# Performance work log

Hardware: AMD Instinct MI355X
Metric: run time of the kernel (lower is better)

## Reference

```python
import jax, jax.numpy as jnp
import numpy as np

B, N, F_IN, F_OUT = 16, 1024, 256, 256
ALPHA = 0.2  # leakyrelu negative slope
NEG_BIG = -9e15


def setup_inputs() -> dict:
    key = jax.random.key(0)
    k1, k2, k3, k4 = jax.random.split(key, 4)
    h = jax.random.normal(k1, (B, N, F_IN), dtype=jnp.float32)
    adj = jax.random.randint(k2, (B, N, N), 0, 2, dtype=jnp.int32)
    # xavier_uniform with gain=1.414
    def xavier(k, shape, gain=1.414):
        fan_in, fan_out = shape[0], shape[1]
        bound = gain * np.sqrt(6.0 / (fan_in + fan_out))
        return jax.random.uniform(k, shape, dtype=jnp.float32, minval=-bound, maxval=bound)
    W = xavier(k3, (F_IN, F_OUT))
    a = xavier(k4, (2 * F_OUT, 1))
    return {"h": h, "adj": adj, "W": W, "a": a}


def reference(h, adj, W, a):
    Wh = jnp.matmul(h, W)  # [B, N, F_OUT]
    # a^T [Wh_i ; Wh_j] = a1^T Wh_i + a2^T Wh_j -- avoids O(N^2 * 2F) concat tensor
    a1 = a[:F_OUT, 0]  # [F_OUT]
    a2 = a[F_OUT:, 0]  # [F_OUT]
    e_i = jnp.einsum('bnf,f->bn', Wh, a1)  # score contribution of source node i
    e_j = jnp.einsum('bnf,f->bn', Wh, a2)  # score contribution of target node j
    e = e_i[:, :, None] + e_j[:, None, :]  # [B, N, N]
    e = jnp.where(e > 0, e, ALPHA * e)  # leaky relu
    e = jnp.where(adj > 0, e, NEG_BIG)
    attention = jax.nn.softmax(e, axis=2)
    h_prime = jnp.matmul(attention, Wh)  # [B, N, F_OUT]
    return jax.nn.elu(h_prime)  # concat=True
```

## Files before the change

kernel.cpp:

```cpp
#include <hip/hip_runtime.h>

#define B_ 16
#define N_ 1024
#define F_ 256
#define ALPHA 0.2f
#define NEG_BIG -9.0e15f

typedef float f4 __attribute__((ext_vector_type(4)));
typedef float f32x4 __attribute__((ext_vector_type(4)));
typedef short s16x8 __attribute__((ext_vector_type(8)));
typedef short s16x4 __attribute__((ext_vector_type(4)));

__device__ inline unsigned short f2b(float x) {
    unsigned int u = __float_as_uint(x);
    u = (u + 0x7FFFu + ((u >> 16) & 1u)) >> 16;
    return (unsigned short)u;
}
__device__ inline float b2f(unsigned short s) {
    unsigned int u = ((unsigned int)s) << 16;
    return __uint_as_float(u);
}

__global__ __launch_bounds__(256) void k_wa(const float* __restrict__ W,
                                            const float* __restrict__ a,
                                            float* __restrict__ wa) {
    __shared__ float sa[512];
    const int t = threadIdx.x, lane = t & 63, w = t >> 6;
    sa[t] = a[t];
    sa[t + 256] = a[t + 256];
    __syncthreads();
    const f4 a1 = *(const f4*)(sa + lane * 4);
    const f4 a2 = *(const f4*)(sa + 256 + lane * 4);
    for (int r = 0; r < 64; ++r) {
        const int row = w * 64 + r;
        const f4 wv = *(const f4*)(W + (size_t)row * F_ + lane * 4);
        float s1 = wv[0]*a1[0] + wv[1]*a1[1] + wv[2]*a1[2] + wv[3]*a1[3];
        float s2 = wv[0]*a2[0] + wv[1]*a2[1] + wv[2]*a2[2] + wv[3]*a2[3];
#pragma unroll
        for (int off = 32; off > 0; off >>= 1) {
            s1 += __shfl_xor(s1, off);
            s2 += __shfl_xor(s2, off);
        }
        if (lane == 0) { wa[row] = s1; wa[256 + row] = s2; }
    }
}

__global__ __launch_bounds__(256) void k_gemm(const float* __restrict__ h,
                                              const float* __restrict__ W,
                                              unsigned short* __restrict__ WhT) {
    __shared__ unsigned short sA[64 * 64];
    __shared__ unsigned short sB[64 * 64];
    const int t = threadIdx.x, l = t & 63, w = t >> 6;
    const int m0 = blockIdx.x * 64, f0 = blockIdx.y * 64;
    const int jg = l >> 4, li = l & 15;
    f32x4 acc[4] = {};

    for (int kt = 0; kt < 4; ++kt) {
        const int k0 = kt * 64;
        if (kt) __syncthreads();
#pragma unroll
        for (int r = 0; r < 2; ++r) {
            const int c = t * 2 + r;
            const int m = c >> 3, kc = c & 7;
            const f4 lo = *(const f4*)(h + (size_t)(m0 + m) * F_ + k0 + kc * 8);
            const f4 hi = *(const f4*)(h + (size_t)(m0 + m) * F_ + k0 + kc * 8 + 4);
            s16x8 v;
            v[0]=(short)f2b(lo[0]); v[1]=(short)f2b(lo[1]); v[2]=(short)f2b(lo[2]); v[3]=(short)f2b(lo[3]);
            v[4]=(short)f2b(hi[0]); v[5]=(short)f2b(hi[1]); v[6]=(short)f2b(hi[2]); v[7]=(short)f2b(hi[3]);
            *(s16x8*)((char*)sA + m * 128 + ((kc ^ (m & 7)) << 4)) = v;
        }
        {
            const int kr = (t >> 4) * 4, fc = (t & 15) * 4;
            f4 r0 = *(const f4*)(W + (size_t)(k0 + kr + 0) * F_ + f0 + fc);
            f4 r1 = *(const f4*)(W + (size_t)(k0 + kr + 1) * F_ + f0 + fc);
            f4 r2 = *(const f4*)(W + (size_t)(k0 + kr + 2) * F_ + f0 + fc);
            f4 r3 = *(const f4*)(W + (size_t)(k0 + kr + 3) * F_ + f0 + fc);
#pragma unroll
            for (int ff = 0; ff < 4; ++ff) {
                const int f = fc + ff;
                s16x4 v;
                v[0]=(short)f2b(r0[ff]); v[1]=(short)f2b(r1[ff]);
                v[2]=(short)f2b(r2[ff]); v[3]=(short)f2b(r3[ff]);
                *(s16x4*)((char*)sB + f * 128 + (((kr >> 3) ^ (f & 7)) << 4) + (kr & 7) * 2) = v;
            }
        }
        __syncthreads();
        const int mloc = w * 16 + li;
#pragma unroll
        for (int ks = 0; ks < 2; ++ks) {
            const int kchunk = ks * 4 + jg;
            const s16x8 av = *(const s16x8*)((const char*)sA + mloc * 128 + ((kchunk ^ (mloc & 7)) << 4));
#pragma unroll
            for (int ft = 0; ft < 4; ++ft) {
                const int f = ft * 16 + li;
                const s16x8 bv = *(const s16x8*)((const char*)sB + f * 128 + ((kchunk ^ (f & 7)) << 4));
                acc[ft] = __builtin_amdgcn_mfma_f32_16x16x32_bf16(av, bv, acc[ft], 0, 0, 0);
            }
        }
    }
    const int bb = m0 >> 10;
    const int mb = (m0 & 1023) + w * 16 + jg * 4;
#pragma unroll
    for (int ft = 0; ft < 4; ++ft) {
        const int fg = f0 + ft * 16 + li;
        s16x4 v;
        v[0]=(short)f2b(acc[ft][0]); v[1]=(short)f2b(acc[ft][1]);
        v[2]=(short)f2b(acc[ft][2]); v[3]=(short)f2b(acc[ft][3]);
        *(s16x4*)(WhT + ((size_t)(bb * 256 + fg)) * 1024 + mb) = v;
    }
}

__global__ __launch_bounds__(256) void k_e2(const float* __restrict__ h,
                                            const float* __restrict__ wa,
                                            float* __restrict__ ei,
                                            float* __restrict__ ej) {
    const int lane = threadIdx.x & 63;
    const int row = blockIdx.x * 4 + (threadIdx.x >> 6);
    const f4 hv = *(const f4*)(h + (size_t)row * F_ + lane * 4);
    const f4 w1 = *(const f4*)(wa + lane * 4);
    const f4 w2 = *(const f4*)(wa + 256 + lane * 4);
    float s1 = hv[0]*w1[0] + hv[1]*w1[1] + hv[2]*w1[2] + hv[3]*w1[3];
    float s2 = hv[0]*w2[0] + hv[1]*w2[1] + hv[2]*w2[2] + hv[3]*w2[3];
#pragma unroll
    for (int off = 32; off > 0; off >>= 1) {
        s1 += __shfl_xor(s1, off);
        s2 += __shfl_xor(s2, off);
    }
    if (lane == 0) { ei[row] = s1; ej[row] = s2; }
}

__global__ __launch_bounds__(256) void k_attn(const unsigned short* __restrict__ WhT,
                                              const float* __restrict__ ei_g,
                                              const float* __restrict__ ej_g,
                                              const int* __restrict__ adj,
                                              float* __restrict__ out) {
    const int id = blockIdx.x;
    const int xcd = id & 7, slot = id >> 3;
    const int b = xcd * 2 + (slot >> 5);
    const int i0 = (slot & 31) * 32;

    __shared__ unsigned short sT[2 * 16384];

    const int t = threadIdx.x, l = t & 63, w = t >> 6;
    const int ih = w >> 1, fbase = (w & 1) * 128;
    const int li = l & 15, jg = l >> 4;
    const int irow = i0 + ih * 16 + li;

    const unsigned short* whb = WhT + (size_t)b * 256 * 1024;
    const int* adjrow = adj + ((size_t)b * N_ + irow) * N_;
    const float* ejb = ej_g + b * N_;
    const float eival = ei_g[b * N_ + irow];

    float m = NEG_BIG, ll = 0.f;
    f32x4 acc[8] = {};

    auto stage = [&](int j0, int buf) {
#pragma unroll
        for (int r = 0; r < 8; ++r) {
            const int c0 = (w * 8 + r) * 64;
            const int c = c0 + l;
            const int f_o = c >> 3, jc_o = c & 7;
            const int jc_s = jc_o ^ (f_o & 7);
            const unsigned short* g = whb + (size_t)f_o * 1024 + j0 + jc_s * 8;
            __builtin_amdgcn_global_load_lds(
                (const __attribute__((address_space(1))) unsigned int*)g,
                (__attribute__((address_space(3))) unsigned int*)((char*)sT + buf * 32768 + c0 * 16),
                16, 0, 0);
        }
    };

    stage(0, 0);
    int4 adjc[4];
#pragma unroll
    for (int q = 0; q < 4; ++q)
        adjc[q] = *(const int4*)(adjrow + (q >> 1) * 32 + jg * 8 + (q & 1) * 4);
    __syncthreads();

    for (int s = 0; s < 16; ++s) {
        const int cur = s & 1;
        int4 adjn[4];
        if (s < 15) {
            const int j0n = (s + 1) * 64;
#pragma unroll
            for (int q = 0; q < 4; ++q)
                adjn[q] = *(const int4*)(adjrow + j0n + (q >> 1) * 32 + jg * 8 + (q & 1) * 4);
        }
#pragma unroll
        for (int sub = 0; sub < 2; ++sub) {
            const int jbase = s * 64 + sub * 32 + jg * 8;
            const f4 ej0 = *(const f4*)(ejb + jbase);
            const f4 ej1 = *(const f4*)(ejb + jbase + 4);
            const int4 a0 = adjc[sub * 2], a1 = adjc[sub * 2 + 1];
            float p[8];
            float tm = NEG_BIG;
#pragma unroll
            for (int e = 0; e < 8; ++e) {
                const float ejv = (e < 4) ? ej0[e] : ej1[e - 4];
                float sc = eival + ejv;
                sc = sc > 0.f ? sc : ALPHA * sc;
                const int ad = (e < 4) ? ((const int*)&a0)[e] : ((const int*)&a1)[e - 4];
                sc = ad > 0 ? sc : NEG_BIG;
                p[e] = sc;
                tm = fmaxf(tm, sc);
            }
            tm = fmaxf(tm, __shfl_xor(tm, 16));
            tm = fmaxf(tm, __shfl_xor(tm, 32));
            if (__any(tm > m + 8.f)) {
                const float mn = fmaxf(m, tm);
                const float fac = __expf(m - mn);
                m = mn;
                ll *= fac;
                float fr[4];
#pragma unroll
                for (int q = 0; q < 4; ++q) fr[q] = __shfl(fac, jg * 4 + q);
#pragma unroll
                for (int ft = 0; ft < 8; ++ft)
#pragma unroll
                    for (int q = 0; q < 4; ++q) acc[ft][q] *= fr[q];
            }
            float sum = 0.f;
            s16x8 afrag;
#pragma unroll
            for (int e = 0; e < 8; ++e) {
                const float pe = __expf(p[e] - m);
                const unsigned short pb = f2b(pe);
                afrag[e] = (short)pb;
                sum += b2f(pb);
            }
            sum += __shfl_xor(sum, 16);
            sum += __shfl_xor(sum, 32);
            ll += sum;
#pragma unroll
            for (int ft = 0; ft < 8; ++ft) {
                const int f = fbase + ft * 16 + li;
                const int jcr = sub * 4 + jg;
                const s16x8 bv = *(const s16x8*)((const char*)sT + cur * 32768 + f * 128 + ((jcr ^ (f & 7)) << 4));
                acc[ft] = __builtin_amdgcn_mfma_f32_16x16x32_bf16(afrag, bv, acc[ft], 0, 0, 0);
            }
        }
        if (s < 15) {
            stage((s + 1) * 64, cur ^ 1);
#pragma unroll
            for (int q = 0; q < 4; ++q) adjc[q] = adjn[q];
        }
        __syncthreads();
    }

    const float il = 1.f / ll;
    float inv[4];
#pragma unroll
    for (int q = 0; q < 4; ++q) inv[q] = __shfl(il, jg * 4 + q);
#pragma unroll
    for (int ft = 0; ft < 8; ++ft) {
#pragma unroll
        for (int q = 0; q < 4; ++q) {
            float v = acc[ft][q] * inv[q];
            v = v > 0.f ? v : __expf(v) - 1.f;
            out[((size_t)b * N_ + i0 + ih * 16 + jg * 4 + q) * F_ + fbase + ft * 16 + li] = v;
        }
    }
}

extern "C" void kernel_launch(void* const* d_in, const int* in_sizes, int n_in,
                              void* d_out, int out_size, void* d_ws, size_t ws_size,
                              hipStream_t stream) {
    const float* h = (const float*)d_in[0];
    const int* adj = (const int*)d_in[1];
    const float* W = (const float*)d_in[2];
    const float* a = (const float*)d_in[3];
    float* out = (float*)d_out;

    unsigned short* WhT = (unsigned short*)d_ws;
    float* wa = (float*)(WhT + (size_t)B_ * N_ * F_);
    float* ei = wa + 512;
    float* ej = ei + (size_t)B_ * N_;

    k_wa<<<1, 256, 0, stream>>>(W, a, wa);
    k_gemm<<<dim3(256, 4), 256, 0, stream>>>(h, W, WhT);
    k_e2<<<(B_ * N_) / 4, 256, 0, stream>>>(h, wa, ei, ej);
    k_attn<<<512, 256, 0, stream>>>(WhT, ei, ej, adj, out);
}
```

Measured before the change: 200.3 us.

## Prefetch next tile earlier, use exp2 softmax, parallelise W·a kernel

Several small tweaks land together. The single-block k_wa kernel now runs on 64 blocks. The attention kernel issues the next tile's global-to-LDS stage before computing the current tile and prefetches ej into registers. Scores are pre-scaled by log2e so the kernel can use exp2 with a raised rescale threshold. Conversions switch to the hip bfloat16 intrinsic, and global addresses are precomputed once. The softmax denominator now sums the fp32 probabilities instead of the rounded bf16 values, and the earlier stage issue may add pressure on the LDS buffer being read.

```diff
diff --git a/kernel.cpp b/kernel.cpp
--- a/kernel.cpp
+++ b/kernel.cpp
@@ -1,48 +1,39 @@
 #include <hip/hip_runtime.h>
+#include <hip/hip_bf16.h>
 
 #define B_ 16
 #define N_ 1024
 #define F_ 256
 #define ALPHA 0.2f
 #define NEG_BIG -9.0e15f
+#define LOG2E 1.4426950408889634f
 
 typedef float f4 __attribute__((ext_vector_type(4)));
 typedef float f32x4 __attribute__((ext_vector_type(4)));
 typedef short s16x8 __attribute__((ext_vector_type(8)));
 typedef short s16x4 __attribute__((ext_vector_type(4)));
 
-__device__ inline unsigned short f2b(float x) {
-    unsigned int u = __float_as_uint(x);
-    u = (u + 0x7FFFu + ((u >> 16) & 1u)) >> 16;
-    return (unsigned short)u;
-}
-__device__ inline float b2f(unsigned short s) {
-    unsigned int u = ((unsigned int)s) << 16;
-    return __uint_as_float(u);
+__device__ inline short f2bs(float x) {
+    __hip_bfloat16 h = __float2bfloat16(x);
+    return __builtin_bit_cast(short, h);
 }
 
 __global__ __launch_bounds__(256) void k_wa(const float* __restrict__ W,
                                             const float* __restrict__ a,
                                             float* __restrict__ wa) {
-    __shared__ float sa[512];
     const int t = threadIdx.x, lane = t & 63, w = t >> 6;
-    sa[t] = a[t];
-    sa[t + 256] = a[t + 256];
-    __syncthreads();
-    const f4 a1 = *(const f4*)(sa + lane * 4);
-    const f4 a2 = *(const f4*)(sa + 256 + lane * 4);
-    for (int r = 0; r < 64; ++r) {
-        const int row = w * 64 + r;
-        const f4 wv = *(const f4*)(W + (size_t)row * F_ + lane * 4);
-        float s1 = wv[0]*a1[0] + wv[1]*a1[1] + wv[2]*a1[2] + wv[3]*a1[3];
-        float s2 = wv[0]*a2[0] + wv[1]*a2[1] + wv[2]*a2[2] + wv[3]*a2[3];
-#pragma unroll
-        for (int off = 32; off > 0; off >>= 1) {
-            s1 += __shfl_xor(s1, off);
-            s2 += __shfl_xor(s2, off);
-        }
-        if (lane == 0) { wa[row] = s1; wa[256 + row] = s2; }
-    }
+    const int row = blockIdx.x * 4 + w;
+    const f4 wv = *(const f4*)(W + (size_t)row * F_ + lane * 4);
+    const f4 a1 = *(const f4*)(a + lane * 4);
+    const f4 a2 = *(const f4*)(a + F_ + lane * 4);
+    float s1 = wv[0]*a1[0] + wv[1]*a1[1] + wv[2]*a1[2] + wv[3]*a1[3];
+    float s2 = wv[0]*a2[0] + wv[1]*a2[1] + wv[2]*a2[2] + wv[3]*a2[3];
+#pragma unroll
+    for (int off = 32; off > 0; off >>= 1) {
+        s1 += __shfl_xor(s1, off);
+        s2 += __shfl_xor(s2, off);
+    }
+    if (lane == 0) { wa[row] = s1; wa[256 + row] = s2; }
 }
 
 __global__ __launch_bounds__(256) void k_gemm(const float* __restrict__ h,
@@ -65,8 +56,8 @@
             const f4 lo = *(const f4*)(h + (size_t)(m0 + m) * F_ + k0 + kc * 8);
             const f4 hi = *(const f4*)(h + (size_t)(m0 + m) * F_ + k0 + kc * 8 + 4);
             s16x8 v;
-            v[0]=(short)f2b(lo[0]); v[1]=(short)f2b(lo[1]); v[2]=(short)f2b(lo[2]); v[3]=(short)f2b(lo[3]);
-            v[4]=(short)f2b(hi[0]); v[5]=(short)f2b(hi[1]); v[6]=(short)f2b(hi[2]); v[7]=(short)f2b(hi[3]);
+            v[0]=f2bs(lo[0]); v[1]=f2bs(lo[1]); v[2]=f2bs(lo[2]); v[3]=f2bs(lo[3]);
+            v[4]=f2bs(hi[0]); v[5]=f2bs(hi[1]); v[6]=f2bs(hi[2]); v[7]=f2bs(hi[3]);
             *(s16x8*)((char*)sA + m * 128 + ((kc ^ (m & 7)) << 4)) = v;
         }
         {
@@ -79,8 +70,7 @@
             for (int ff = 0; ff < 4; ++ff) {
                 const int f = fc + ff;
                 s16x4 v;
-                v[0]=(short)f2b(r0[ff]); v[1]=(short)f2b(r1[ff]);
-                v[2]=(short)f2b(r2[ff]); v[3]=(short)f2b(r3[ff]);
+                v[0]=f2bs(r0[ff]); v[1]=f2bs(r1[ff]); v[2]=f2bs(r2[ff]); v[3]=f2bs(r3[ff]);
                 *(s16x4*)((char*)sB + f * 128 + (((kr >> 3) ^ (f & 7)) << 4) + (kr & 7) * 2) = v;
             }
         }
@@ -104,8 +94,8 @@
     for (int ft = 0; ft < 4; ++ft) {
         const int fg = f0 + ft * 16 + li;
         s16x4 v;
-        v[0]=(short)f2b(acc[ft][0]); v[1]=(short)f2b(acc[ft][1]);
-        v[2]=(short)f2b(acc[ft][2]); v[3]=(short)f2b(acc[ft][3]);
+        v[0]=f2bs(acc[ft][0]); v[1]=f2bs(acc[ft][1]);
+        v[2]=f2bs(acc[ft][2]); v[3]=f2bs(acc[ft][3]);
         *(s16x4*)(WhT + ((size_t)(bb * 256 + fg)) * 1024 + mb) = v;
     }
 }
@@ -126,7 +116,7 @@
         s1 += __shfl_xor(s1, off);
         s2 += __shfl_xor(s2, off);
     }
-    if (lane == 0) { ei[row] = s1; ej[row] = s2; }
+    if (lane == 0) { ei[row] = s1 * LOG2E; ej[row] = s2 * LOG2E; }
 }
 
 __global__ __launch_bounds__(256) void k_attn(const unsigned short* __restrict__ WhT,
@@ -146,50 +136,61 @@
     const int li = l & 15, jg = l >> 4;
     const int irow = i0 + ih * 16 + li;
 
-    const unsigned short* whb = WhT + (size_t)b * 256 * 1024;
+    const unsigned short* whb = WhT + (size_t)b * F_ * N_;
     const int* adjrow = adj + ((size_t)b * N_ + irow) * N_;
     const float* ejb = ej_g + b * N_;
     const float eival = ei_g[b * N_ + irow];
 
+    const unsigned short* gsrc[8];
+    int ldst[8];
+#pragma unroll
+    for (int r = 0; r < 8; ++r) {
+        const int c0 = (w * 8 + r) * 64;
+        const int c = c0 + l;
+        const int f_o = c >> 3;
+        const int jc_s = (c & 7) ^ (f_o & 7);
+        gsrc[r] = whb + (size_t)f_o * N_ + jc_s * 8;
+        ldst[r] = c0 * 16;
+    }
+    auto stage = [&](int j0, int buf) {
+#pragma unroll
+        for (int r = 0; r < 8; ++r) {
+            __builtin_amdgcn_global_load_lds(
+                (const __attribute__((address_space(1))) unsigned int*)(gsrc[r] + j0),
+                (__attribute__((address_space(3))) unsigned int*)((char*)sT + buf * 32768 + ldst[r]),
+                16, 0, 0);
+        }
+    };
+
     float m = NEG_BIG, ll = 0.f;
     f32x4 acc[8] = {};
 
-    auto stage = [&](int j0, int buf) {
-#pragma unroll
-        for (int r = 0; r < 8; ++r) {
-            const int c0 = (w * 8 + r) * 64;
-            const int c = c0 + l;
-            const int f_o = c >> 3, jc_o = c & 7;
-            const int jc_s = jc_o ^ (f_o & 7);
-            const unsigned short* g = whb + (size_t)f_o * 1024 + j0 + jc_s * 8;
-            __builtin_amdgcn_global_load_lds(
-                (const __attribute__((address_space(1))) unsigned int*)g,
-                (__attribute__((address_space(3))) unsigned int*)((char*)sT + buf * 32768 + c0 * 16),
-                16, 0, 0);
-        }
-    };
-
     stage(0, 0);
     int4 adjc[4];
-#pragma unroll
-    for (int q = 0; q < 4; ++q)
+    f4 ejc[4];
+#pragma unroll
+    for (int q = 0; q < 4; ++q) {
         adjc[q] = *(const int4*)(adjrow + (q >> 1) * 32 + jg * 8 + (q & 1) * 4);
+        ejc[q] = *(const f4*)(ejb + (q >> 1) * 32 + jg * 8 + (q & 1) * 4);
+    }
     __syncthreads();
 
     for (int s = 0; s < 16; ++s) {
         const int cur = s & 1;
         int4 adjn[4];
+        f4 ejn[4];
         if (s < 15) {
+            stage((s + 1) * 64, cur ^ 1);
             const int j0n = (s + 1) * 64;
 #pragma unroll
-            for (int q = 0; q < 4; ++q)
+            for (int q = 0; q < 4; ++q) {
                 adjn[q] = *(const int4*)(adjrow + j0n + (q >> 1) * 32 + jg * 8 + (q & 1) * 4);
+                ejn[q] = *(const f4*)(ejb + j0n + (q >> 1) * 32 + jg * 8 + (q & 1) * 4);
+            }
         }
 #pragma unroll
         for (int sub = 0; sub < 2; ++sub) {
-            const int jbase = s * 64 + sub * 32 + jg * 8;
-            const f4 ej0 = *(const f4*)(ejb + jbase);
-            const f4 ej1 = *(const f4*)(ejb + jbase + 4);
+            const f4 ej0 = ejc[sub * 2], ej1 = ejc[sub * 2 + 1];
             const int4 a0 = adjc[sub * 2], a1 = adjc[sub * 2 + 1];
             float p[8];
             float tm = NEG_BIG;
@@ -197,7 +198,7 @@
             for (int e = 0; e < 8; ++e) {
                 const float ejv = (e < 4) ? ej0[e] : ej1[e - 4];
                 float sc = eival + ejv;
-                sc = sc > 0.f ? sc : ALPHA * sc;
+                sc = fmaxf(sc, ALPHA * sc);
                 const int ad = (e < 4) ? ((const int*)&a0)[e] : ((const int*)&a1)[e - 4];
                 sc = ad > 0 ? sc : NEG_BIG;
                 p[e] = sc;
@@ -205,9 +206,9 @@
             }
             tm = fmaxf(tm, __shfl_xor(tm, 16));
             tm = fmaxf(tm, __shfl_xor(tm, 32));
-            if (__any(tm > m + 8.f)) {
+            if (__any(tm > m + 11.5f)) {
                 const float mn = fmaxf(m, tm);
-                const float fac = __expf(m - mn);
+                const float fac = __builtin_amdgcn_exp2f(m - mn);
                 m = mn;
                 ll *= fac;
                 float fr[4];
@@ -222,10 +223,9 @@
             s16x8 afrag;
 #pragma unroll
             for (int e = 0; e < 8; ++e) {
-                const float pe = __expf(p[e] - m);
-                const unsigned short pb = f2b(pe);
-                afrag[e] = (short)pb;
-                sum += b2f(pb);
+                const float pe = __builtin_amdgcn_exp2f(p[e] - m);
+                afrag[e] = f2bs(pe);
+                sum += pe;
             }
             sum += __shfl_xor(sum, 16);
             sum += __shfl_xor(sum, 32);
@@ -239,9 +239,8 @@
             }
         }
         if (s < 15) {
-            stage((s + 1) * 64, cur ^ 1);
-#pragma unroll
-            for (int q = 0; q < 4; ++q) adjc[q] = adjn[q];
+#pragma unroll
+            for (int q = 0; q < 4; ++q) { adjc[q] = adjn[q]; ejc[q] = ejn[q]; }
         }
         __syncthreads();
     }
@@ -255,7 +254,7 @@
 #pragma unroll
         for (int q = 0; q < 4; ++q) {
             float v = acc[ft][q] * inv[q];
-            v = v > 0.f ? v : __expf(v) - 1.f;
+            v = v > 0.f ? v : __builtin_amdgcn_exp2f(v * LOG2E) - 1.f;
             out[((size_t)b * N_ + i0 + ih * 16 + jg * 4 + q) * F_ + fbase + ft * 16 + li] = v;
         }
     }
@@ -275,7 +274,7 @@
     float* ei = wa + 512;
     float* ej = ei + (size_t)B_ * N_;
 
-    k_wa<<<1, 256, 0, stream>>>(W, a, wa);
+    k_wa<<<64, 256, 0, stream>>>(W, a, wa);
     k_gemm<<<dim3(256, 4), 256, 0, stream>>>(h, W, WhT);
     k_e2<<<(B_ * N_) / 4, 256, 0, stream>>>(h, wa, ei, ej);
     k_attn<<<512, 256, 0, stream>>>(WhT, ei, ej, adj, out);
```

Result: faster. 160.9 us (-19.6%).
